# Kernel tuning notes

Measured on AMD Instinct MI355X. Metric: run time of the kernel, lower is better.

The kernel has to match this reference:

```python
import jax, jax.numpy as jnp
import numpy as np

TIM_SIZE, TIM_EMB = 48, 64
APP_SIZE, APP_EMB = 10000, 256
UID_SIZE, UID_EMB = 10000, 256
INPUT_SIZE = TIM_EMB + APP_EMB  # 320
S = 4096
N = S - 3  # windows of length 4


def setup_inputs() -> dict:
    key = jax.random.key(0)
    ks = jax.random.split(key, 12)
    inp = {
        "tim": jax.random.randint(ks[0], (S, 1), 0, TIM_SIZE),
        "app": jax.random.uniform(ks[1], (S, APP_SIZE), dtype=jnp.float32),
        "loc": jax.random.randint(ks[2], (S, 1), 0, 1),
        "uid": jax.random.randint(ks[3], (1,), 0, UID_SIZE),
        "ptim": jax.random.randint(ks[4], (N, 1), 0, TIM_SIZE),
        # learned parameters
        "emb_tim_w": jax.random.normal(ks[5], (TIM_SIZE, TIM_EMB), dtype=jnp.float32) * 0.02,
        "emb_uid_w": jax.random.normal(ks[6], (UID_SIZE, UID_EMB), dtype=jnp.float32) * 0.02,
        "emb_app_w": jax.random.normal(ks[7], (APP_SIZE, APP_EMB), dtype=jnp.float32) * 0.02,
        "attn_W": jax.random.uniform(ks[8], (INPUT_SIZE, 1), dtype=jnp.float32),
        "attn_b": jax.random.uniform(ks[9], (4, 1), dtype=jnp.float32),
        "attn_fc_w": jax.random.normal(ks[10], (APP_EMB, INPUT_SIZE), dtype=jnp.float32) * 0.02,
        "attn_fc_b": jnp.zeros((APP_EMB,), dtype=jnp.float32),
        "dec_w": jax.random.normal(ks[11], (APP_SIZE, APP_EMB + TIM_EMB), dtype=jnp.float32) * 0.02,
        "dec_b": jnp.zeros((APP_SIZE,), dtype=jnp.float32),
    }
    return inp


def reference(tim, app, loc, uid, ptim, emb_tim_w, emb_uid_w, emb_app_w,
              attn_W, attn_b, attn_fc_w, attn_fc_b, dec_w, dec_b):
    # embeddings (squeeze(1) in torch)
    tim_emb = emb_tim_w[tim[:, 0]]    # [S, TIM_EMB]
    ptim_emb = emb_tim_w[ptim[:, 0]]  # [N, TIM_EMB]
    # 'sum' app embedding mode: multi-hot @ table
    app_emb = app @ emb_app_w         # [S, APP_EMB]
    x = jnp.concatenate([app_emb, tim_emb], axis=1)  # [S, INPUT_SIZE]; dropout is identity at eval
    # sliding windows of length 4 (vectorizes the torch per-i loop)
    n = tim.shape[0] - 3
    idx = jnp.arange(n)[:, None] + jnp.arange(4)[None, :]  # [N, 4]
    win = x[idx]                                          # [N, 4, INPUT_SIZE]
    H = jnp.tanh(win @ attn_W + attn_b)                   # [N, 4, 1]
    Xn = H / jnp.sum(jnp.abs(H), axis=(1, 2), keepdims=True)  # L1 normalize over the window
    pooled = jnp.einsum('nf,nfd->nd', Xn[:, :, 0], win)   # [N, INPUT_SIZE]
    out = pooled @ attn_fc_w.T + attn_fc_b                # [N, APP_EMB]
    uid_emb = emb_uid_w[uid[0]]                           # [APP_EMB], broadcast = repeat
    out = out * uid_emb
    out = jnp.concatenate([out, ptim_emb], axis=1)        # [N, APP_EMB+TIM_EMB]
    score = jax.nn.sigmoid(out @ dec_w.T + dec_b)         # [N, APP_SIZE]
    return score
```

## Files before the change

### kernel.cpp

```cpp
#include <hip/hip_runtime.h>

typedef __attribute__((ext_vector_type(8))) short  bf16x8;
typedef __attribute__((ext_vector_type(8))) unsigned short u16x8;
typedef __attribute__((ext_vector_type(4))) float  f32x4;

constexpr int S    = 4096;
constexpr int NR   = 4093;
constexpr int KAPP = 10000;
constexpr int KPAD = 10112;
constexpr int EAPP = 256;
constexpr int ETIM = 64;
constexpr int DIN  = 320;
constexpr int NDEC = 10000;
constexpr int LDP  = 40;

__device__ inline unsigned short f2bf(float f) {
    unsigned u = __float_as_uint(f);
    u += 0x7fffu + ((u >> 16) & 1u);
    return (unsigned short)(u >> 16);
}
__device__ inline float bf2f(unsigned short h) {
    return __uint_as_float(((unsigned)h) << 16);
}
__device__ inline u16x8 pack8(f32x4 a, f32x4 b) {
    u16x8 v;
    v[0]=f2bf(a.x); v[1]=f2bf(a.y); v[2]=f2bf(a.z); v[3]=f2bf(a.w);
    v[4]=f2bf(b.x); v[5]=f2bf(b.y); v[6]=f2bf(b.z); v[7]=f2bf(b.w);
    return v;
}

__global__ __launch_bounds__(256) void k_cvt_bf16(
    const float* __restrict__ in, unsigned short* __restrict__ out, int n8)
{
    int id = blockIdx.x * 256 + threadIdx.x;
    if (id >= n8) return;
    const float* p = in + (size_t)id * 8;
    f32x4 a = *reinterpret_cast<const f32x4*>(p);
    f32x4 b = *reinterpret_cast<const f32x4*>(p + 4);
    *reinterpret_cast<u16x8*>(out + (size_t)id * 8) = pack8(a, b);
}

__global__ __launch_bounds__(256) void k_transpose_appw(
    const float* __restrict__ B, unsigned short* __restrict__ Bp)
{
    __shared__ float T[64][68];
    const int kt = blockIdx.x * 64, nt = blockIdx.y * 64;
    const int tid = threadIdx.x;
    #pragma unroll
    for (int i = 0; i < 4; ++i) {
        int c = tid + (i << 8);
        int k = c >> 4, n4 = (c & 15) << 2;
        f32x4 v = {0.f, 0.f, 0.f, 0.f};
        if (kt + k < KAPP)
            v = *reinterpret_cast<const f32x4*>(&B[(size_t)(kt + k) * EAPP + nt + n4]);
        *reinterpret_cast<f32x4*>(&T[k][n4]) = v;
    }
    __syncthreads();
    #pragma unroll
    for (int i = 0; i < 2; ++i) {
        int c = tid + (i << 8);
        int n = c >> 3, ko = (c & 7) << 3;
        u16x8 v;
        #pragma unroll
        for (int j = 0; j < 8; ++j) v[j] = f2bf(T[ko + j][n]);
        *reinterpret_cast<u16x8*>(&Bp[(size_t)(nt + n) * KPAD + kt + ko]) = v;
    }
}

__global__ __launch_bounds__(256) void k_embed_tim(
    const int* __restrict__ tim, const float* __restrict__ emb_tim,
    unsigned short* __restrict__ xb)
{
    int r = blockIdx.x * 4 + (threadIdx.x >> 6);
    int e = threadIdx.x & 63;
    xb[(size_t)r * DIN + EAPP + e] = f2bf(emb_tim[tim[r] * ETIM + e]);
}
__global__ __launch_bounds__(256) void k_embed_ptim(
    const int* __restrict__ ptim, const float* __restrict__ emb_tim,
    unsigned short* __restrict__ yb)
{
    int r = blockIdx.x * 4 + (threadIdx.x >> 6);
    int e = threadIdx.x & 63;
    if (r < NR) yb[(size_t)r * DIN + EAPP + e] = f2bf(emb_tim[ptim[r] * ETIM + e]);
}

__global__ __launch_bounds__(256) void k_gemm_app_mfma(
    const float* __restrict__ A, const unsigned short* __restrict__ Bp,
    float* __restrict__ part)
{
    __shared__ unsigned short As[2][64 * LDP];
    __shared__ unsigned short Bs[2][256 * LDP];
    const int tid = threadIdx.x;
    const int lane = tid & 63, w = tid >> 6;
    const int ks = blockIdx.x;
    const int bm = blockIdx.y << 6;
    const int k0 = ks * 2528;

    u16x8 ra, rb[4];
    auto gload = [&](int kt) {
        {
            int row = tid >> 2, ko = (tid & 3) << 3;
            int k = kt + ko;
            u16x8 v = {0,0,0,0,0,0,0,0};
            if (k < KAPP) {
                const float* p = &A[(size_t)(bm + row) * KAPP + k];
                v = pack8(*reinterpret_cast<const f32x4*>(p),
                          *reinterpret_cast<const f32x4*>(p + 4));
            }
            ra = v;
        }
        #pragma unroll
        for (int i = 0; i < 4; ++i) {
            int c = tid + (i << 8);
            int n = c >> 2, ko = (c & 3) << 3;
            rb[i] = *reinterpret_cast<const u16x8*>(&Bp[(size_t)n * KPAD + kt + ko]);
        }
    };
    auto swrite = [&](int b) {
        {
            int row = tid >> 2, ko = (tid & 3) << 3;
            *reinterpret_cast<u16x8*>(&As[b][row * LDP + ko]) = ra;
        }
        #pragma unroll
        for (int i = 0; i < 4; ++i) {
            int c = tid + (i << 8);
            int n = c >> 2, ko = (c & 3) << 3;
            *reinterpret_cast<u16x8*>(&Bs[b][n * LDP + ko]) = rb[i];
        }
    };

    f32x4 zero = {0.f, 0.f, 0.f, 0.f};
    f32x4 acc[4][4];
    #pragma unroll
    for (int i = 0; i < 4; ++i)
        #pragma unroll
        for (int j = 0; j < 4; ++j) acc[i][j] = zero;

    constexpr int NS = 79;
    gload(k0); swrite(0); __syncthreads();
    for (int s = 0; s < NS; ++s) {
        int cur = s & 1;
        if (s + 1 < NS) gload(k0 + ((s + 1) << 5));
        const int kh8 = (lane >> 4) << 3, rl = lane & 15;
        bf16x8 af[4], bfr[4];
        #pragma unroll
        for (int i = 0; i < 4; ++i)
            af[i] = *reinterpret_cast<const bf16x8*>(&As[cur][(i * 16 + rl) * LDP + kh8]);
        #pragma unroll
        for (int j = 0; j < 4; ++j)
            bfr[j] = *reinterpret_cast<const bf16x8*>(&Bs[cur][((w << 6) + j * 16 + rl) * LDP + kh8]);
        #pragma unroll
        for (int i = 0; i < 4; ++i)
            #pragma unroll
            for (int j = 0; j < 4; ++j)
                acc[i][j] = __builtin_amdgcn_mfma_f32_16x16x32_bf16(af[i], bfr[j], acc[i][j], 0, 0, 0);
        if (s + 1 < NS) {
            __syncthreads();
            swrite(cur ^ 1);
            __syncthreads();
        }
    }
    float* P = part + ((size_t)ks * S + bm) * EAPP;
    const int rq = (lane >> 4) << 2, rl = lane & 15;
    #pragma unroll
    for (int i = 0; i < 4; ++i)
        #pragma unroll
        for (int j = 0; j < 4; ++j) {
            int col = (w << 6) + j * 16 + rl;
            #pragma unroll
            for (int q = 0; q < 4; ++q)
                P[(size_t)(i * 16 + rq + q) * EAPP + col] = acc[i][j][q];
        }
}

__global__ __launch_bounds__(256) void k_reduce_app(
    const float* __restrict__ part, unsigned short* __restrict__ xb)
{
    int id = blockIdx.x * 256 + threadIdx.x;
    int row = id >> 6, c4 = (id & 63) << 2;
    f32x4 s = {0.f, 0.f, 0.f, 0.f};
    #pragma unroll
    for (int sl = 0; sl < 4; ++sl) {
        f32x4 v = *reinterpret_cast<const f32x4*>(
            &part[((size_t)sl * S + row) * EAPP + c4]);
        s.x += v.x; s.y += v.y; s.z += v.z; s.w += v.w;
    }
    unsigned short* o = &xb[(size_t)row * DIN + c4];
    o[0] = f2bf(s.x); o[1] = f2bf(s.y); o[2] = f2bf(s.z); o[3] = f2bf(s.w);
}

__global__ __launch_bounds__(256) void k_score(
    const unsigned short* __restrict__ xb, const float* __restrict__ W,
    float* __restrict__ s)
{
    int wv = threadIdx.x >> 6, lane = threadIdx.x & 63;
    int m = blockIdx.x * 4 + wv;
    float sum = 0.f;
    #pragma unroll
    for (int i = 0; i < 5; ++i) {
        int k = lane + (i << 6);
        sum += bf2f(xb[(size_t)m * DIN + k]) * W[k];
    }
    #pragma unroll
    for (int off = 32; off; off >>= 1) sum += __shfl_down(sum, off);
    if (lane == 0) s[m] = sum;
}

__global__ void k_pooled(
    const unsigned short* __restrict__ xb, const float* __restrict__ s,
    const float* __restrict__ attn_b, unsigned short* __restrict__ pooledb)
{
    int n = blockIdx.x, d = threadIdx.x;
    float h[4], den = 0.f;
    #pragma unroll
    for (int f = 0; f < 4; ++f) {
        h[f] = tanhf(s[n + f] + attn_b[f]);
        den += fabsf(h[f]);
    }
    float inv = 1.f / den, p = 0.f;
    #pragma unroll
    for (int f = 0; f < 4; ++f)
        p = fmaf(h[f] * inv, bf2f(xb[(size_t)(n + f) * DIN + d]), p);
    pooledb[(size_t)n * DIN + d] = f2bf(p);
}

template<int EPI>
__global__ __launch_bounds__(256) void k_gemm_nt_mfma(
    const unsigned short* __restrict__ A, const unsigned short* __restrict__ B,
    int Nb, int K, int Mlim,
    const float* __restrict__ bias,
    const float* __restrict__ emb_uid, const int* __restrict__ uid,
    void* __restrict__ Cout, int ldc)
{
    __shared__ unsigned short As[2][128 * LDP];
    __shared__ unsigned short Bs[2][128 * LDP];
    const int tid = threadIdx.x;
    const int lane = tid & 63, w = tid >> 6;
    const int bn = blockIdx.x << 7, bm = blockIdx.y << 7;
    const int wr = (w >> 1) << 6, wc = (w & 1) << 6;

    u16x8 ra[2], rb[2];
    auto gload = [&](int kt) {
        #pragma unroll
        for (int i = 0; i < 2; ++i) {
            int c = tid + (i << 8);
            int row = c >> 2, ko = (c & 3) << 3;
            ra[i] = *reinterpret_cast<const u16x8*>(&A[(size_t)(bm + row) * K + kt + ko]);
            int brow = bn + row;
            u16x8 z = {0,0,0,0,0,0,0,0};
            rb[i] = (brow < Nb)
                ? *reinterpret_cast<const u16x8*>(&B[(size_t)brow * K + kt + ko]) : z;
        }
    };
    auto swrite = [&](int b) {
        #pragma unroll
        for (int i = 0; i < 2; ++i) {
            int c = tid + (i << 8);
            int row = c >> 2, ko = (c & 3) << 3;
            *reinterpret_cast<u16x8*>(&As[b][row * LDP + ko]) = ra[i];
            *reinterpret_cast<u16x8*>(&Bs[b][row * LDP + ko]) = rb[i];
        }
    };

    f32x4 zero = {0.f, 0.f, 0.f, 0.f};
    f32x4 acc[4][4];
    #pragma unroll
    for (int i = 0; i < 4; ++i)
        #pragma unroll
        for (int j = 0; j < 4; ++j) acc[i][j] = zero;

    const int NS = K >> 5;
    gload(0); swrite(0); __syncthreads();
    for (int s = 0; s < NS; ++s) {
        int cur = s & 1;
        if (s + 1 < NS) gload((s + 1) << 5);
        const int kh8 = (lane >> 4) << 3, rl = lane & 15;
        bf16x8 af[4], bfr[4];
        #pragma unroll
        for (int i = 0; i < 4; ++i)
            af[i] = *reinterpret_cast<const bf16x8*>(&As[cur][(wr + i * 16 + rl) * LDP + kh8]);
        #pragma unroll
        for (int j = 0; j < 4; ++j)
            bfr[j] = *reinterpret_cast<const bf16x8*>(&Bs[cur][(wc + j * 16 + rl) * LDP + kh8]);
        #pragma unroll
        for (int i = 0; i < 4; ++i)
            #pragma unroll
            for (int j = 0; j < 4; ++j)
                acc[i][j] = __builtin_amdgcn_mfma_f32_16x16x32_bf16(af[i], bfr[j], acc[i][j], 0, 0, 0);
        if (s + 1 < NS) {
            __syncthreads();
            swrite(cur ^ 1);
            __syncthreads();
        }
    }

    const int rq = (lane >> 4) << 2, rl = lane & 15;
    if (EPI == 1) {
        unsigned short* C = (unsigned short*)Cout;
        const float* us = emb_uid + (size_t)uid[0] * EAPP;
        #pragma unroll
        for (int j = 0; j < 4; ++j) {
            int col = bn + wc + j * 16 + rl;
            float um = us[col], bb = bias[col];
            #pragma unroll
            for (int i = 0; i < 4; ++i)
                #pragma unroll
                for (int q = 0; q < 4; ++q) {
                    int row = bm + wr + i * 16 + rq + q;
                    C[(size_t)row * ldc + col] = f2bf((acc[i][j][q] + bb) * um);
                }
        }
    } else {
        float* C = (float*)Cout;
        #pragma unroll
        for (int j = 0; j < 4; ++j) {
            int col = bn + wc + j * 16 + rl;
            if (col >= Nb) continue;
            float bb = bias[col];
            #pragma unroll
            for (int i = 0; i < 4; ++i)
                #pragma unroll
                for (int q = 0; q < 4; ++q) {
                    int row = bm + wr + i * 16 + rq + q;
                    if (row < Mlim) {
                        float v = acc[i][j][q] + bb;
                        C[(size_t)row * ldc + col] = 1.f / (1.f + __expf(-v));
                    }
                }
        }
    }
}

extern "C" void kernel_launch(void* const* d_in, const int* in_sizes, int n_in,
                              void* d_out, int out_size, void* d_ws, size_t ws_size,
                              hipStream_t stream)
{
    const int*   tim       = (const int*)  d_in[0];
    const float* app       = (const float*)d_in[1];
    const int*   uid       = (const int*)  d_in[3];
    const int*   ptim      = (const int*)  d_in[4];
    const float* emb_tim_w = (const float*)d_in[5];
    const float* emb_uid_w = (const float*)d_in[6];
    const float* emb_app_w = (const float*)d_in[7];
    const float* attn_W    = (const float*)d_in[8];
    const float* attn_b    = (const float*)d_in[9];
    const float* attn_fc_w = (const float*)d_in[10];
    const float* attn_fc_b = (const float*)d_in[11];
    const float* dec_w     = (const float*)d_in[12];
    const float* dec_b     = (const float*)d_in[13];
    float* out = (float*)d_out;

    char* w = (char*)d_ws;
    size_t o = 0;
    auto alloc = [&](size_t bytes) { char* p = w + o; o = (o + bytes + 511) & ~(size_t)511; return p; };
    unsigned short* xb      = (unsigned short*)alloc((size_t)S * DIN * 2);
    unsigned short* pooledb = (unsigned short*)alloc((size_t)S * DIN * 2);
    unsigned short* yb      = (unsigned short*)alloc((size_t)S * DIN * 2);
    float*          s       = (float*)        alloc((size_t)S * 4);
    unsigned short* Bp      = (unsigned short*)alloc((size_t)EAPP * KPAD * 2);
    unsigned short* decb    = (unsigned short*)alloc((size_t)NDEC * DIN * 2);
    unsigned short* fcb     = (unsigned short*)alloc((size_t)EAPP * DIN * 2);
    float*          part    = (float*)        alloc((size_t)4 * S * EAPP * 4);

    k_cvt_bf16<<<(NDEC * DIN / 8 + 255) / 256, 256, 0, stream>>>(dec_w, decb, NDEC * DIN / 8);
    k_cvt_bf16<<<(EAPP * DIN / 8 + 255) / 256, 256, 0, stream>>>(attn_fc_w, fcb, EAPP * DIN / 8);
    dim3 gT(KPAD / 64, EAPP / 64);
    k_transpose_appw<<<gT, 256, 0, stream>>>(emb_app_w, Bp);
    k_embed_tim<<<S / 4, 256, 0, stream>>>(tim, emb_tim_w, xb);

    dim3 gApp(4, S / 64);
    k_gemm_app_mfma<<<gApp, 256, 0, stream>>>(app, Bp, part);
    k_reduce_app<<<S * 64 / 256, 256, 0, stream>>>(part, xb);

    k_score<<<S / 4, 256, 0, stream>>>(xb, attn_W, s);
    k_pooled<<<NR, DIN, 0, stream>>>(xb, s, attn_b, pooledb);
    k_embed_ptim<<<S / 4, 256, 0, stream>>>(ptim, emb_tim_w, yb);

    dim3 gFc(EAPP / 128, S / 128);
    k_gemm_nt_mfma<1><<<gFc, 256, 0, stream>>>(pooledb, fcb, EAPP, DIN, S,
                                               attn_fc_b, emb_uid_w, uid, yb, DIN);
    dim3 gDec((NDEC + 127) / 128, S / 128);
    k_gemm_nt_mfma<2><<<gDec, 256, 0, stream>>>(yb, decb, NDEC, DIN, NR,
                                                dec_b, nullptr, nullptr, out, NDEC);
}
```

Measured before the change: 241.2 us.

## Drop LDS staging in all GEMMs, load MFMA fragments directly from global

Rewrites the app-embedding GEMM and the two NT GEMMs to load MFMA operand fragments straight from global memory into registers, with no shared-memory double buffering and no __syncthreads. The app GEMM split-K goes from 4 to 8 chunks, each with a tail step, and the reduce kernel now sums 8 partials. This removes LDS traffic and barrier stalls, but each wave now reloads fragments that other waves in the block also read. Every wave of the block issues separate global loads of the 64-row fp32 A tile. The result relies on L1/L2 to absorb the redundancy and adds more partial-sum traffic.

```diff
diff --git a/kernel.cpp b/kernel.cpp
--- a/kernel.cpp
+++ b/kernel.cpp
@@ -12,7 +12,8 @@
 constexpr int ETIM = 64;
 constexpr int DIN  = 320;
 constexpr int NDEC = 10000;
-constexpr int LDP  = 40;
+constexpr int NSK  = 8;
+constexpr int KCH  = 1256;
 
 __device__ inline unsigned short f2bf(float f) {
     unsigned u = __float_as_uint(f);
@@ -27,6 +28,9 @@
     v[0]=f2bf(a.x); v[1]=f2bf(a.y); v[2]=f2bf(a.z); v[3]=f2bf(a.w);
     v[4]=f2bf(b.x); v[5]=f2bf(b.y); v[6]=f2bf(b.z); v[7]=f2bf(b.w);
     return v;
+}
+__device__ inline bf16x8 as_bf(u16x8 v) {
+    union { u16x8 u; bf16x8 b; } c; c.u = v; return c.b;
 }
 
 __global__ __launch_bounds__(256) void k_cvt_bf16(
@@ -84,89 +88,66 @@
     if (r < NR) yb[(size_t)r * DIN + EAPP + e] = f2bf(emb_tim[ptim[r] * ETIM + e]);
 }
 
-__global__ __launch_bounds__(256) void k_gemm_app_mfma(
+template<bool TAIL>
+__device__ __forceinline__ void app_step(
     const float* __restrict__ A, const unsigned short* __restrict__ Bp,
-    float* __restrict__ part)
-{
-    __shared__ unsigned short As[2][64 * LDP];
-    __shared__ unsigned short Bs[2][256 * LDP];
-    const int tid = threadIdx.x;
-    const int lane = tid & 63, w = tid >> 6;
-    const int ks = blockIdx.x;
-    const int bm = blockIdx.y << 6;
-    const int k0 = ks * 2528;
-
-    u16x8 ra, rb[4];
-    auto gload = [&](int kt) {
-        {
-            int row = tid >> 2, ko = (tid & 3) << 3;
-            int k = kt + ko;
+    int kt, int kend, int bm, int wc, int rl, int kh8, f32x4 (&acc)[4][4])
+{
+    #pragma unroll
+    for (int h = 0; h < 2; ++h) {
+        const int kg = kt + h * 32 + kh8;
+        bf16x8 af[4], bfr[4];
+        #pragma unroll
+        for (int i = 0; i < 4; ++i) {
             u16x8 v = {0,0,0,0,0,0,0,0};
-            if (k < KAPP) {
-                const float* p = &A[(size_t)(bm + row) * KAPP + k];
+            if (!TAIL || kg + 8 <= kend) {
+                const float* p = A + (size_t)(bm + i * 16 + rl) * KAPP + kg;
                 v = pack8(*reinterpret_cast<const f32x4*>(p),
                           *reinterpret_cast<const f32x4*>(p + 4));
             }
-            ra = v;
-        }
-        #pragma unroll
-        for (int i = 0; i < 4; ++i) {
-            int c = tid + (i << 8);
-            int n = c >> 2, ko = (c & 3) << 3;
-            rb[i] = *reinterpret_cast<const u16x8*>(&Bp[(size_t)n * KPAD + kt + ko]);
-        }
-    };
-    auto swrite = [&](int b) {
-        {
-            int row = tid >> 2, ko = (tid & 3) << 3;
-            *reinterpret_cast<u16x8*>(&As[b][row * LDP + ko]) = ra;
-        }
-        #pragma unroll
-        for (int i = 0; i < 4; ++i) {
-            int c = tid + (i << 8);
-            int n = c >> 2, ko = (c & 3) << 3;
-            *reinterpret_cast<u16x8*>(&Bs[b][n * LDP + ko]) = rb[i];
-        }
-    };
-
-    f32x4 zero = {0.f, 0.f, 0.f, 0.f};
+            af[i] = as_bf(v);
+        }
+        #pragma unroll
+        for (int j = 0; j < 4; ++j)
+            bfr[j] = *reinterpret_cast<const bf16x8*>(
+                &Bp[(size_t)(wc + j * 16 + rl) * KPAD + kg]);
+        #pragma unroll
+        for (int i = 0; i < 4; ++i)
+            #pragma unroll
+            for (int j = 0; j < 4; ++j)
+                acc[i][j] = __builtin_amdgcn_mfma_f32_16x16x32_bf16(
+                    af[i], bfr[j], acc[i][j], 0, 0, 0);
+    }
+}
+
+__global__ __launch_bounds__(256) void k_gemm_app_direct(
+    const float* __restrict__ A, const unsigned short* __restrict__ Bp,
+    float* __restrict__ part)
+{
+    const int tid = threadIdx.x, lane = tid & 63, w = tid >> 6;
+    const int ks = blockIdx.x, bm = blockIdx.y << 6;
+    const int wc = w << 6, rl = lane & 15, kh8 = (lane >> 4) << 3;
+    const int k0 = ks * KCH;
+    const int kend = min(k0 + KCH, KAPP);
+    const int nfull = (kend - k0) >> 6;
+
     f32x4 acc[4][4];
     #pragma unroll
     for (int i = 0; i < 4; ++i)
         #pragma unroll
-        for (int j = 0; j < 4; ++j) acc[i][j] = zero;
-
-    constexpr int NS = 79;
-    gload(k0); swrite(0); __syncthreads();
-    for (int s = 0; s < NS; ++s) {
-        int cur = s & 1;
-        if (s + 1 < NS) gload(k0 + ((s + 1) << 5));
-        const int kh8 = (lane >> 4) << 3, rl = lane & 15;
-        bf16x8 af[4], bfr[4];
-        #pragma unroll
-        for (int i = 0; i < 4; ++i)
-            af[i] = *reinterpret_cast<const bf16x8*>(&As[cur][(i * 16 + rl) * LDP + kh8]);
-        #pragma unroll
-        for (int j = 0; j < 4; ++j)
-            bfr[j] = *reinterpret_cast<const bf16x8*>(&Bs[cur][((w << 6) + j * 16 + rl) * LDP + kh8]);
-        #pragma unroll
-        for (int i = 0; i < 4; ++i)
-            #pragma unroll
-            for (int j = 0; j < 4; ++j)
-                acc[i][j] = __builtin_amdgcn_mfma_f32_16x16x32_bf16(af[i], bfr[j], acc[i][j], 0, 0, 0);
-        if (s + 1 < NS) {
-            __syncthreads();
-            swrite(cur ^ 1);
-            __syncthreads();
-        }
-    }
+        for (int j = 0; j < 4; ++j) acc[i][j] = (f32x4){0.f, 0.f, 0.f, 0.f};
+
+    for (int s = 0; s < nfull; ++s)
+        app_step<false>(A, Bp, k0 + (s << 6), kend, bm, wc, rl, kh8, acc);
+    app_step<true>(A, Bp, k0 + (nfull << 6), kend, bm, wc, rl, kh8, acc);
+
     float* P = part + ((size_t)ks * S + bm) * EAPP;
-    const int rq = (lane >> 4) << 2, rl = lane & 15;
+    const int rq = (lane >> 4) << 2;
     #pragma unroll
     for (int i = 0; i < 4; ++i)
         #pragma unroll
         for (int j = 0; j < 4; ++j) {
-            int col = (w << 6) + j * 16 + rl;
+            int col = wc + j * 16 + rl;
             #pragma unroll
             for (int q = 0; q < 4; ++q)
                 P[(size_t)(i * 16 + rq + q) * EAPP + col] = acc[i][j][q];
@@ -180,7 +161,7 @@
     int row = id >> 6, c4 = (id & 63) << 2;
     f32x4 s = {0.f, 0.f, 0.f, 0.f};
     #pragma unroll
-    for (int sl = 0; sl < 4; ++sl) {
+    for (int sl = 0; sl < NSK; ++sl) {
         f32x4 v = *reinterpret_cast<const f32x4*>(
             &part[((size_t)sl * S + row) * EAPP + c4]);
         s.x += v.x; s.y += v.y; s.z += v.z; s.w += v.w;
@@ -225,76 +206,52 @@
 }
 
 template<int EPI>
-__global__ __launch_bounds__(256) void k_gemm_nt_mfma(
+__global__ __launch_bounds__(256) void k_gemm_nt_direct(
     const unsigned short* __restrict__ A, const unsigned short* __restrict__ B,
-    int Nb, int K, int Mlim,
+    int Nb, int Mlim,
     const float* __restrict__ bias,
     const float* __restrict__ emb_uid, const int* __restrict__ uid,
     void* __restrict__ Cout, int ldc)
 {
-    __shared__ unsigned short As[2][128 * LDP];
-    __shared__ unsigned short Bs[2][128 * LDP];
-    const int tid = threadIdx.x;
-    const int lane = tid & 63, w = tid >> 6;
+    const int tid = threadIdx.x, lane = tid & 63, w = tid >> 6;
     const int bn = blockIdx.x << 7, bm = blockIdx.y << 7;
     const int wr = (w >> 1) << 6, wc = (w & 1) << 6;
-
-    u16x8 ra[2], rb[2];
-    auto gload = [&](int kt) {
-        #pragma unroll
-        for (int i = 0; i < 2; ++i) {
-            int c = tid + (i << 8);
-            int row = c >> 2, ko = (c & 3) << 3;
-            ra[i] = *reinterpret_cast<const u16x8*>(&A[(size_t)(bm + row) * K + kt + ko]);
-            int brow = bn + row;
-            u16x8 z = {0,0,0,0,0,0,0,0};
-            rb[i] = (brow < Nb)
-                ? *reinterpret_cast<const u16x8*>(&B[(size_t)brow * K + kt + ko]) : z;
-        }
-    };
-    auto swrite = [&](int b) {
-        #pragma unroll
-        for (int i = 0; i < 2; ++i) {
-            int c = tid + (i << 8);
-            int row = c >> 2, ko = (c & 3) << 3;
-            *reinterpret_cast<u16x8*>(&As[b][row * LDP + ko]) = ra[i];
-            *reinterpret_cast<u16x8*>(&Bs[b][row * LDP + ko]) = rb[i];
-        }
-    };
-
-    f32x4 zero = {0.f, 0.f, 0.f, 0.f};
+    const int rl = lane & 15, kh8 = (lane >> 4) << 3;
+
     f32x4 acc[4][4];
     #pragma unroll
     for (int i = 0; i < 4; ++i)
         #pragma unroll
-        for (int j = 0; j < 4; ++j) acc[i][j] = zero;
-
-    const int NS = K >> 5;
-    gload(0); swrite(0); __syncthreads();
-    for (int s = 0; s < NS; ++s) {
-        int cur = s & 1;
-        if (s + 1 < NS) gload((s + 1) << 5);
-        const int kh8 = (lane >> 4) << 3, rl = lane & 15;
-        bf16x8 af[4], bfr[4];
-        #pragma unroll
-        for (int i = 0; i < 4; ++i)
-            af[i] = *reinterpret_cast<const bf16x8*>(&As[cur][(wr + i * 16 + rl) * LDP + kh8]);
-        #pragma unroll
-        for (int j = 0; j < 4; ++j)
-            bfr[j] = *reinterpret_cast<const bf16x8*>(&Bs[cur][(wc + j * 16 + rl) * LDP + kh8]);
-        #pragma unroll
-        for (int i = 0; i < 4; ++i)
-            #pragma unroll
-            for (int j = 0; j < 4; ++j)
-                acc[i][j] = __builtin_amdgcn_mfma_f32_16x16x32_bf16(af[i], bfr[j], acc[i][j], 0, 0, 0);
-        if (s + 1 < NS) {
-            __syncthreads();
-            swrite(cur ^ 1);
-            __syncthreads();
-        }
-    }
-
-    const int rq = (lane >> 4) << 2, rl = lane & 15;
+        for (int j = 0; j < 4; ++j) acc[i][j] = (f32x4){0.f, 0.f, 0.f, 0.f};
+
+    #pragma unroll
+    for (int s = 0; s < DIN / 64; ++s) {
+        #pragma unroll
+        for (int h = 0; h < 2; ++h) {
+            const int kg = (s << 6) + h * 32 + kh8;
+            bf16x8 af[4], bfr[4];
+            #pragma unroll
+            for (int i = 0; i < 4; ++i)
+                af[i] = *reinterpret_cast<const bf16x8*>(
+                    &A[(size_t)(bm + wr + i * 16 + rl) * DIN + kg]);
+            #pragma unroll
+            for (int j = 0; j < 4; ++j) {
+                int brow = bn + wc + j * 16 + rl;
+                u16x8 v = {0,0,0,0,0,0,0,0};
+                if (brow < Nb)
+                    v = *reinterpret_cast<const u16x8*>(&B[(size_t)brow * DIN + kg]);
+                bfr[j] = as_bf(v);
+            }
+            #pragma unroll
+            for (int i = 0; i < 4; ++i)
+                #pragma unroll
+                for (int j = 0; j < 4; ++j)
+                    acc[i][j] = __builtin_amdgcn_mfma_f32_16x16x32_bf16(
+                        af[i], bfr[j], acc[i][j], 0, 0, 0);
+        }
+    }
+
+    const int rq = (lane >> 4) << 2;
     if (EPI == 1) {
         unsigned short* C = (unsigned short*)Cout;
         const float* us = emb_uid + (size_t)uid[0] * EAPP;
@@ -360,7 +317,7 @@
     unsigned short* Bp      = (unsigned short*)alloc((size_t)EAPP * KPAD * 2);
     unsigned short* decb    = (unsigned short*)alloc((size_t)NDEC * DIN * 2);
     unsigned short* fcb     = (unsigned short*)alloc((size_t)EAPP * DIN * 2);
-    float*          part    = (float*)        alloc((size_t)4 * S * EAPP * 4);
+    float*          part    = (float*)        alloc((size_t)NSK * S * EAPP * 4);
 
     k_cvt_bf16<<<(NDEC * DIN / 8 + 255) / 256, 256, 0, stream>>>(dec_w, decb, NDEC * DIN / 8);
     k_cvt_bf16<<<(EAPP * DIN / 8 + 255) / 256, 256, 0, stream>>>(attn_fc_w, fcb, EAPP * DIN / 8);
@@ -368,8 +325,8 @@
     k_transpose_appw<<<gT, 256, 0, stream>>>(emb_app_w, Bp);
     k_embed_tim<<<S / 4, 256, 0, stream>>>(tim, emb_tim_w, xb);
 
-    dim3 gApp(4, S / 64);
-    k_gemm_app_mfma<<<gApp, 256, 0, stream>>>(app, Bp, part);
+    dim3 gApp(NSK, S / 64);
+    k_gemm_app_direct<<<gApp, 256, 0, stream>>>(app, Bp, part);
     k_reduce_app<<<S * 64 / 256, 256, 0, stream>>>(part, xb);
 
     k_score<<<S / 4, 256, 0, stream>>>(xb, attn_W, s);
@@ -377,9 +334,9 @@
     k_embed_ptim<<<S / 4, 256, 0, stream>>>(ptim, emb_tim_w, yb);
 
     dim3 gFc(EAPP / 128, S / 128);
-    k_gemm_nt_mfma<1><<<gFc, 256, 0, stream>>>(pooledb, fcb, EAPP, DIN, S,
-                                               attn_fc_b, emb_uid_w, uid, yb, DIN);
+    k_gemm_nt_direct<1><<<gFc, 256, 0, stream>>>(pooledb, fcb, EAPP, S,
+                                                 attn_fc_b, emb_uid_w, uid, yb, DIN);
     dim3 gDec((NDEC + 127) / 128, S / 128);
-    k_gemm_nt_mfma<2><<<gDec, 256, 0, stream>>>(yb, decb, NDEC, DIN, NR,
-                                                dec_b, nullptr, nullptr, out, NDEC);
-}
+    k_gemm_nt_direct<2><<<gDec, 256, 0, stream>>>(yb, decb, NDEC, NR,
+                                                  dec_b, nullptr, nullptr, out, NDEC);
+}
```

Result: slower. 316.3 us (+31.2%).
